# Kernel tuning notes

Hardware: AMD Instinct MI355X
Metric: run time of the kernel (lower is better)

Reference implementation:

```python
import jax, jax.numpy as jnp
import numpy as np
from jax import lax

B, T, I, H = 64, 512, 512, 1024


def setup_inputs() -> dict:
    key = jax.random.key(0)
    k1, k2, k3, k4 = jax.random.split(key, 4)
    # Gates stacked in order: resetgate, updategate, hidden_update (matches forward()).
    inp = jax.random.normal(k1, (B, T, I), dtype=jnp.float32)
    W_in_stacked = jax.random.normal(k2, (I, 3 * H), dtype=jnp.float32) * 0.1
    W_hid_stacked = jax.random.normal(k3, (H, 3 * H), dtype=jnp.float32) * 0.1
    b_stacked = jax.random.normal(k4, (3 * H,), dtype=jnp.float32) * 0.1
    hid_init = jnp.zeros((1, H), dtype=jnp.float32)
    return {"inp": inp, "W_in_stacked": W_in_stacked,
            "W_hid_stacked": W_hid_stacked, "b_stacked": b_stacked,
            "hid_init": hid_init}


def reference(inp, W_in_stacked, W_hid_stacked, b_stacked, hid_init):
    n_units = hid_init.shape[1]
    n_batch = inp.shape[0]
    # Precompute the input contribution for all timesteps (as the original does
    # with one big mm before the loop): [B,T,3H] -> [T,B,3H] seq-first.
    x = jnp.einsum('bti,ig->btg', inp, W_in_stacked) + b_stacked
    x = jnp.swapaxes(x, 0, 1)
    h0 = jnp.broadcast_to(hid_init, (n_batch, n_units))

    def step(h_prev, x_t):
        hid_input = h_prev @ W_hid_stacked  # [B, 3H]
        r = jax.nn.sigmoid(x_t[:, :n_units] + hid_input[:, :n_units])
        u = jax.nn.sigmoid(x_t[:, n_units:2 * n_units]
                           + hid_input[:, n_units:2 * n_units])
        c = jnp.tanh(x_t[:, 2 * n_units:] + r * hid_input[:, 2 * n_units:])
        h_new = (1.0 - u) * h_prev + u * c
        return h_new, None

    h_final, _ = lax.scan(step, h0, x)
    return h_final  # [B, n_units]
```

## Files before the change

kernel.cpp:

```cpp
#include <hip/hip_runtime.h>
#include <hip/hip_fp16.h>
#include <math.h>

typedef _Float16 h16;
typedef __attribute__((ext_vector_type(4))) _Float16 h16x4;
typedef __attribute__((ext_vector_type(8))) _Float16 h16x8;
typedef __attribute__((ext_vector_type(4))) float f32x4;
typedef unsigned long long u64;

#define T_SEQ 512
#define NB    64
#define NI    512
#define NH    1024
#define N3H   3072

#define TAGM 0x0001000100010001ULL

__device__ __forceinline__ u64 cload64(const u64* p) {
  return __hip_atomic_load(p, __ATOMIC_RELAXED, __HIP_MEMORY_SCOPE_AGENT);
}
__device__ __forceinline__ void cstore64(u64* p, u64 v) {
  __hip_atomic_store(p, v, __ATOMIC_RELAXED, __HIP_MEMORY_SCOPE_AGENT);
}

union H4 { u64 q; h16x4 v; };
union F8 { u64 q[2]; h16x8 v; };

__device__ __forceinline__ u64 tagpat(unsigned e) {
  return (u64)(e & 1) | ((u64)((e >> 1) & 1) << 16)
       | ((u64)((e >> 2) & 1) << 32) | ((u64)((e >> 3) & 1) << 48);
}


__global__ void gru_init_h(const float* __restrict__ hid0,
                           u64* __restrict__ hfrag) {
  int W = blockIdx.x * blockDim.x + threadIdx.x;
  if (W >= 16384) return;
  int bg = W >> 12;
  int w  = W & 4095;
  int kt = w >> 7;
  int lp = (w >> 1) & 63;
  int q  = w & 1;
  int cb = kt * 32 + (lp >> 4) * 8 + q * 4;
  H4 o;
  #pragma unroll
  for (int j = 0; j < 4; ++j) o.v[j] = (h16)hid0[cb + j];
  hfrag[(size_t)bg * 4096 + w] = o.q & ~TAGM;
}

#define P1_BM 128
#define P1_BK 32

__device__ __forceinline__ int p1swz(int r, int k) {
  return r * P1_BK + ((((k >> 3) ^ (r & 3)) << 3) | (k & 7));
}

__global__ __launch_bounds__(256, 2) void gru_xgemm(
    const float* __restrict__ inp, const float* __restrict__ Win,
    const float* __restrict__ bstk, h16* __restrict__ x) {
  __shared__ h16 sAh[2][P1_BM * P1_BK];
  __shared__ h16 sAl[2][P1_BM * P1_BK];
  __shared__ h16 sBh[2][P1_BM * P1_BK];
  __shared__ h16 sBl[2][P1_BM * P1_BK];

  const int tid = threadIdx.x;
  const int l = tid & 63;
  const int w = tid >> 6;
  const int wm = (w >> 1) * 64, wn = (w & 1) * 64;
  const int mi = blockIdx.x, ni = blockIdx.y;

  const int sr  = tid >> 1;
  const int skh = (tid & 1) * 16;

  const float* aSrcBase = inp + (size_t)(sr & 63) * (T_SEQ * NI)
                              + (size_t)(mi * 2 + (sr >> 6)) * NI + skh;
  const float* bSrcBase = Win + (size_t)skh * N3H + ni * 128 + sr;

  f32x4 acc[4][4] = {};
  float aReg[16];
  float bReg[16];

  auto stage_load = [&](int ks) {
    const float* ap = aSrcBase + ks * P1_BK;
    #pragma unroll
    for (int jg = 0; jg < 4; ++jg) {
      f32x4 v = *(const f32x4*)(ap + jg * 4);
      aReg[jg*4+0] = v[0]; aReg[jg*4+1] = v[1];
      aReg[jg*4+2] = v[2]; aReg[jg*4+3] = v[3];
    }
    const float* bp = bSrcBase + (size_t)ks * P1_BK * N3H;
    #pragma unroll
    for (int j = 0; j < 16; ++j) bReg[j] = bp[(size_t)j * N3H];
  };

  auto stage_write = [&](int buf) {
    #pragma unroll
    for (int jg = 0; jg < 4; ++jg) {
      int idx = p1swz(sr, skh + jg * 4);
      h16x4 hi, lo;
      #pragma unroll
      for (int j = 0; j < 4; ++j) {
        float v = aReg[jg*4+j];
        h16 h = (h16)v; hi[j] = h; lo[j] = (h16)(v - (float)h);
      }
      *(h16x4*)&sAh[buf][idx] = hi;
      *(h16x4*)&sAl[buf][idx] = lo;
      #pragma unroll
      for (int j = 0; j < 4; ++j) {
        float v = bReg[jg*4+j];
        h16 h = (h16)v; hi[j] = h; lo[j] = (h16)(v - (float)h);
      }
      *(h16x4*)&sBh[buf][idx] = hi;
      *(h16x4*)&sBl[buf][idx] = lo;
    }
  };

  auto compute = [&](int buf) {
    const int k0 = (l >> 4) * 8;
    h16x8 bh[4], bl[4];
    #pragma unroll
    for (int nt = 0; nt < 4; ++nt) {
      int idx = p1swz(wn + nt * 16 + (l & 15), k0);
      bh[nt] = *(const h16x8*)&sBh[buf][idx];
      bl[nt] = *(const h16x8*)&sBl[buf][idx];
    }
    #pragma unroll
    for (int mt = 0; mt < 4; ++mt) {
      int idx = p1swz(wm + mt * 16 + (l & 15), k0);
      h16x8 ah = *(const h16x8*)&sAh[buf][idx];
      h16x8 al = *(const h16x8*)&sAl[buf][idx];
      #pragma unroll
      for (int nt = 0; nt < 4; ++nt) {
        acc[mt][nt] = __builtin_amdgcn_mfma_f32_16x16x32_f16(ah, bh[nt], acc[mt][nt], 0, 0, 0);
        acc[mt][nt] = __builtin_amdgcn_mfma_f32_16x16x32_f16(ah, bl[nt], acc[mt][nt], 0, 0, 0);
        acc[mt][nt] = __builtin_amdgcn_mfma_f32_16x16x32_f16(al, bh[nt], acc[mt][nt], 0, 0, 0);
      }
    }
  };

  stage_load(0);
  stage_write(0);
  __syncthreads();
  for (int ks = 0; ks < 16; ++ks) {
    int buf = ks & 1;
    if (ks < 15) stage_load(ks + 1);
    compute(buf);
    if (ks < 15) stage_write(buf ^ 1);
    __syncthreads();
  }

  const int t = mi * 2 + (wm >> 6);
  const int rrb = (l >> 4) * 4;
  #pragma unroll
  for (int nt = 0; nt < 4; ++nt) {
    int colhi = ni * 8 + (wn >> 4) + nt;
    int gg  = colhi >> 6;
    int cgx = colhi & 63;
    float bias = bstk[(colhi << 4) + (l & 15)];
    #pragma unroll
    for (int mt = 0; mt < 4; ++mt) {
      h16x4 v;
      #pragma unroll
      for (int i = 0; i < 4; ++i) v[i] = (h16)(acc[mt][nt][i] + bias);
      size_t idx = ((((size_t)t * 3 + gg) * 64 + cgx) * 4 + mt) * 256
                 + (size_t)(l & 15) * 16 + rrb;
      *(h16x4*)&x[idx] = v;
    }
  }
}

__global__ __launch_bounds__(192, 1) void gru_steps(
    const float* __restrict__ Whid,
    const h16* __restrict__ x,
    u64* __restrict__ hfrag,
    const float* __restrict__ hid0,
    float* __restrict__ out) {
  __shared__ h16 U[3 * 32 * 64 * 8];
  __shared__ h16 tq[16 * 20];

  const int tid = threadIdx.x;
  const int l = tid & 63;
  const int g = tid >> 6;
  const int cg = blockIdx.x & 63;
  const int bg = blockIdx.x >> 6;

  {
    const float* base = Whid + (size_t)g * NH + (size_t)cg * 16 + (l & 15);
    for (int kt = 0; kt < 32; ++kt) {
      const float* src = base + (size_t)(kt * 32 + (l >> 4) * 8) * N3H;
      h16x8 v;
      #pragma unroll
      for (int j = 0; j < 8; ++j) v[j] = (h16)src[(size_t)j * N3H];
      *(h16x8*)&U[(size_t)((g * 32 + kt) * 64 + l) * 8] = v;
    }
  }
  __syncthreads();
  if (g != 0) return;

  const int rr0 = (l >> 4) * 4, cc = l & 15;

  float hq[4];
  {
    float h0 = hid0[cg * 16 + cc];
    #pragma unroll
    for (int i = 0; i < 4; ++i) hq[i] = h0;
  }

  const char* xb0 = (const char*)(x + ((((size_t)0 * 64 + cg) * 4 + bg) * 256)
                                    + (size_t)cc * 16 + rr0);
  const char* xb1 = xb0 + 64 * 4 * 256 * 2;
  const char* xb2 = xb1 + 64 * 4 * 256 * 2;
  u64 xq0 = *(const u64*)xb0, xq1 = *(const u64*)xb1, xq2 = *(const u64*)xb2;

  const int dstw = cg * 64 + ((l >> 4) >> 1) * 32 + (l & 15) * 2 + ((l >> 4) & 1);

  for (int s = 1; s <= T_SEQ; ++s) {
    const u64* plane = hfrag + ((size_t)((s - 1) & 1) * 4 + bg) * 4096;
    const u64 patc = tagpat((((unsigned)(s - 1)) >> 1) & 15u);

    u64 xn0 = xq0, xn1 = xq1, xn2 = xq2;
    if (s < T_SEQ) {
      xn0 = *(const u64*)(xb0 + (size_t)s * 393216);
      xn1 = *(const u64*)(xb1 + (size_t)s * 393216);
      xn2 = *(const u64*)(xb2 + (size_t)s * 393216);
    }

    f32x4 ac0 = {}, ac1 = {}, ac2 = {};
    u64 w0[16], w1[16], w2[16], w3[16];

    auto loadc = [&](u64 (&W)[16], int c) {
      #pragma unroll
      for (int j = 0; j < 16; ++j) {
        int kt = c * 8 + (j >> 1);
        W[j] = cload64(plane + ((size_t)kt * 64 + l) * 2 + (j & 1));
      }
    };
    auto fixc = [&](u64 (&W)[16], int c) {
      for (int tries = 0; tries < 30000; ++tries) {
        unsigned bad = 0;
        #pragma unroll
        for (int j = 0; j < 16; ++j)
          bad |= (((W[j] ^ patc) & TAGM) != 0ULL) ? (1u << j) : 0u;
        if (bad == 0) break;
        if (tries > 4) __builtin_amdgcn_s_sleep(1);
        #pragma unroll
        for (int j = 0; j < 16; ++j) {
          int kt = c * 8 + (j >> 1);
          if (bad & (1u << j))
            W[j] = cload64(plane + ((size_t)kt * 64 + l) * 2 + (j & 1));
        }
      }
    };
    auto mfmac = [&](u64 (&W)[16], int c) {
      #pragma unroll
      for (int j = 0; j < 8; ++j) {
        int kt = c * 8 + j;
        F8 f; f.q[0] = W[2 * j]; f.q[1] = W[2 * j + 1];
        h16x8 b0 = *(const h16x8*)&U[(size_t)((0 * 32 + kt) * 64 + l) * 8];
        h16x8 b1 = *(const h16x8*)&U[(size_t)((1 * 32 + kt) * 64 + l) * 8];
        h16x8 b2 = *(const h16x8*)&U[(size_t)((2 * 32 + kt) * 64 + l) * 8];
        ac0 = __builtin_amdgcn_mfma_f32_16x16x32_f16(f.v, b0, ac0, 0, 0, 0);
        ac1 = __builtin_amdgcn_mfma_f32_16x16x32_f16(f.v, b1, ac1, 0, 0, 0);
        ac2 = __builtin_amdgcn_mfma_f32_16x16x32_f16(f.v, b2, ac2, 0, 0, 0);
      }
    };

    loadc(w0, 0);
    loadc(w1, 1);
    fixc(w0, 0);
    loadc(w2, 2);
    mfmac(w0, 0);
    fixc(w1, 1);
    loadc(w3, 3);
    mfmac(w1, 1);
    fixc(w2, 2);
    mfmac(w2, 2);
    fixc(w3, 3);
    mfmac(w3, 3);

    H4 xr; xr.q = xq0;
    H4 xu; xu.q = xq1;
    H4 xc; xc.q = xq2;
    #pragma unroll
    for (int i = 0; i < 4; ++i) {
      float r = 1.0f / (1.0f + __expf(-((float)xr.v[i] + ac0[i])));
      float u = 1.0f / (1.0f + __expf(-((float)xu.v[i] + ac1[i])));
      float z = (float)xc.v[i] + r * ac2[i];
      float e = __expf(2.0f * z);
      float c = 1.0f - 2.0f / (e + 1.0f);
      float hn = (1.0f - u) * hq[i] + u * c;
      hq[i] = hn;
      tq[(rr0 + i) * 20 + cc] = (h16)hn;
      if (s == T_SEQ) out[(size_t)(bg * 16 + rr0 + i) * NH + cg * 16 + cc] = hn;
    }

    H4 pv; pv.v = *(const h16x4*)&tq[(l & 15) * 20 + (l >> 4) * 4];
    u64 word = (pv.q & ~TAGM) | tagpat(((unsigned)s >> 1) & 15u);
    u64* outp = hfrag + ((size_t)(s & 1) * 4 + bg) * 4096;
    cstore64(outp + dstw, word);

    xq0 = xn0; xq1 = xn1; xq2 = xn2;
  }
}

extern "C" void kernel_launch(void* const* d_in, const int* in_sizes, int n_in,
                              void* d_out, int out_size, void* d_ws, size_t ws_size,
                              hipStream_t stream) {
  const float* inp  = (const float*)d_in[0];
  const float* Win  = (const float*)d_in[1];
  const float* Whid = (const float*)d_in[2];
  const float* bstk = (const float*)d_in[3];
  const float* hid0 = (const float*)d_in[4];
  float* out = (float*)d_out;

  char* ws = (char*)d_ws;
  const size_t xBytes = (size_t)T_SEQ * NB * N3H * sizeof(h16);
  const size_t hBytes = (size_t)2 * 4 * 4096 * sizeof(u64);
  if (ws_size < xBytes + hBytes) return;

  h16* x = (h16*)ws;
  u64* hfrag = (u64*)(ws + xBytes);

  gru_init_h<<<dim3(16384 / 256), dim3(256), 0, stream>>>(hid0, hfrag);

  dim3 g1(32768 / P1_BM, N3H / 128);
  gru_xgemm<<<g1, dim3(256), 0, stream>>>(inp, Win, bstk, x);

  gru_steps<<<dim3(256), dim3(192), 0, stream>>>(Whid, x, hfrag, hid0, out);
}
```

Baseline: 2.663 ms.

## Use 128-bit coherent loads with manual vmcnt pipelining for hidden-state exchange

Polls of the cross-block hidden-state fragments now use 16-byte global_load_dwordx4 with sc0 sc1 cache bypass instead of pairs of 8-byte atomic loads. Explicit s_waitcnt vmcnt barriers stage the four chunk loads so fewer words are in flight, and the per-step x prefetch moves to the end of the step so it no longer occupies the vmcnt counter during polling. The aim is to cut the number of memory instructions and the latency on the recurrent critical path. The hand-written asm and waitcnt counts depend on exact instruction ordering, so a miscount could consume stale data or stall.

```diff
diff --git a/kernel.cpp b/kernel.cpp
--- a/kernel.cpp
+++ b/kernel.cpp
@@ -6,6 +6,7 @@
 typedef __attribute__((ext_vector_type(4))) _Float16 h16x4;
 typedef __attribute__((ext_vector_type(8))) _Float16 h16x8;
 typedef __attribute__((ext_vector_type(4))) float f32x4;
+typedef __attribute__((ext_vector_type(4))) unsigned u32x4;
 typedef unsigned long long u64;
 
 #define T_SEQ 512
@@ -22,9 +23,18 @@
 __device__ __forceinline__ void cstore64(u64* p, u64 v) {
   __hip_atomic_store(p, v, __ATOMIC_RELAXED, __HIP_MEMORY_SCOPE_AGENT);
 }
+__device__ __forceinline__ u32x4 cload128(const u64* p) {
+  u32x4 v;
+  asm volatile("global_load_dwordx4 %0, %1, off sc0 sc1" : "=v"(v) : "v"(p));
+  return v;
+}
+#define VMWAIT(N) do { \
+  asm volatile("s_waitcnt vmcnt(" #N ")" ::: "memory"); \
+  __builtin_amdgcn_sched_barrier(0); \
+} while (0)
 
 union H4 { u64 q; h16x4 v; };
-union F8 { u64 q[2]; h16x8 v; };
+union F16B { u32x4 d; u64 q[2]; h16x8 v; };
 
 __device__ __forceinline__ u64 tagpat(unsigned e) {
   return (u64)(e & 1) | ((u64)((e >> 1) & 1) << 16)
@@ -214,69 +224,65 @@
 
   const int dstw = cg * 64 + ((l >> 4) >> 1) * 32 + (l & 15) * 2 + ((l >> 4) & 1);
 
+  VMWAIT(0);
+
   for (int s = 1; s <= T_SEQ; ++s) {
     const u64* plane = hfrag + ((size_t)((s - 1) & 1) * 4 + bg) * 4096;
     const u64 patc = tagpat((((unsigned)(s - 1)) >> 1) & 15u);
 
-    u64 xn0 = xq0, xn1 = xq1, xn2 = xq2;
-    if (s < T_SEQ) {
-      xn0 = *(const u64*)(xb0 + (size_t)s * 393216);
-      xn1 = *(const u64*)(xb1 + (size_t)s * 393216);
-      xn2 = *(const u64*)(xb2 + (size_t)s * 393216);
-    }
-
     f32x4 ac0 = {}, ac1 = {}, ac2 = {};
-    u64 w0[16], w1[16], w2[16], w3[16];
-
-    auto loadc = [&](u64 (&W)[16], int c) {
-      #pragma unroll
-      for (int j = 0; j < 16; ++j) {
-        int kt = c * 8 + (j >> 1);
-        W[j] = cload64(plane + ((size_t)kt * 64 + l) * 2 + (j & 1));
-      }
+    F16B W0[8], W1[8], W2[8];
+
+    auto issue = [&](F16B (&W)[8], int c) {
+      #pragma unroll
+      for (int j = 0; j < 8; ++j)
+        W[j].d = cload128(plane + ((size_t)(c * 8 + j) * 64 + l) * 2);
     };
-    auto fixc = [&](u64 (&W)[16], int c) {
+    auto fix = [&](F16B (&W)[8], int c) {
       for (int tries = 0; tries < 30000; ++tries) {
         unsigned bad = 0;
         #pragma unroll
-        for (int j = 0; j < 16; ++j)
-          bad |= (((W[j] ^ patc) & TAGM) != 0ULL) ? (1u << j) : 0u;
+        for (int j = 0; j < 8; ++j)
+          bad |= ((((W[j].q[0] ^ patc) | (W[j].q[1] ^ patc)) & TAGM) != 0ULL)
+                   ? (1u << j) : 0u;
         if (bad == 0) break;
         if (tries > 4) __builtin_amdgcn_s_sleep(1);
         #pragma unroll
-        for (int j = 0; j < 16; ++j) {
-          int kt = c * 8 + (j >> 1);
+        for (int j = 0; j < 8; ++j)
           if (bad & (1u << j))
-            W[j] = cload64(plane + ((size_t)kt * 64 + l) * 2 + (j & 1));
-        }
+            W[j].d = cload128(plane + ((size_t)(c * 8 + j) * 64 + l) * 2);
+        VMWAIT(0);
       }
     };
-    auto mfmac = [&](u64 (&W)[16], int c) {
+    auto mfmac = [&](F16B (&W)[8], int c) {
       #pragma unroll
       for (int j = 0; j < 8; ++j) {
         int kt = c * 8 + j;
-        F8 f; f.q[0] = W[2 * j]; f.q[1] = W[2 * j + 1];
         h16x8 b0 = *(const h16x8*)&U[(size_t)((0 * 32 + kt) * 64 + l) * 8];
         h16x8 b1 = *(const h16x8*)&U[(size_t)((1 * 32 + kt) * 64 + l) * 8];
         h16x8 b2 = *(const h16x8*)&U[(size_t)((2 * 32 + kt) * 64 + l) * 8];
-        ac0 = __builtin_amdgcn_mfma_f32_16x16x32_f16(f.v, b0, ac0, 0, 0, 0);
-        ac1 = __builtin_amdgcn_mfma_f32_16x16x32_f16(f.v, b1, ac1, 0, 0, 0);
-        ac2 = __builtin_amdgcn_mfma_f32_16x16x32_f16(f.v, b2, ac2, 0, 0, 0);
+        ac0 = __builtin_amdgcn_mfma_f32_16x16x32_f16(W[j].v, b0, ac0, 0, 0, 0);
+        ac1 = __builtin_amdgcn_mfma_f32_16x16x32_f16(W[j].v, b1, ac1, 0, 0, 0);
+        ac2 = __builtin_amdgcn_mfma_f32_16x16x32_f16(W[j].v, b2, ac2, 0, 0, 0);
       }
     };
 
-    loadc(w0, 0);
-    loadc(w1, 1);
-    fixc(w0, 0);
-    loadc(w2, 2);
-    mfmac(w0, 0);
-    fixc(w1, 1);
-    loadc(w3, 3);
-    mfmac(w1, 1);
-    fixc(w2, 2);
-    mfmac(w2, 2);
-    fixc(w3, 3);
-    mfmac(w3, 3);
+    issue(W0, 0);
+    issue(W1, 1);
+    VMWAIT(8);
+    fix(W0, 0);
+    issue(W2, 2);
+    mfmac(W0, 0);
+    issue(W0, 3);
+    VMWAIT(16);
+    fix(W1, 1);
+    mfmac(W1, 1);
+    VMWAIT(8);
+    fix(W2, 2);
+    mfmac(W2, 2);
+    VMWAIT(0);
+    fix(W0, 3);
+    mfmac(W0, 3);
 
     H4 xr; xr.q = xq0;
     H4 xu; xu.q = xq1;
@@ -299,7 +305,11 @@
     u64* outp = hfrag + ((size_t)(s & 1) * 4 + bg) * 4096;
     cstore64(outp + dstw, word);
 
-    xq0 = xn0; xq1 = xn1; xq2 = xn2;
+    if (s < T_SEQ) {
+      xq0 = *(const u64*)(xb0 + (size_t)s * 393216);
+      xq1 = *(const u64*)(xb1 + (size_t)s * 393216);
+      xq2 = *(const u64*)(xb2 + (size_t)s * 393216);
+    }
   }
 }
 
```

After: 2.807 ms. +5.4%, slower.
